# Kernel tuning notes

Hardware: AMD Instinct MI355X
Metric: run time of the kernel (lower is better)

Reference implementation:

```python
import jax, jax.numpy as jnp
import numpy as np

B, N, GN, GS = 16, 100000, 4096, 64  # batch, points, num_groups, group_size


def setup_inputs() -> dict:
    key = jax.random.key(0)
    k1, k2, k3 = jax.random.split(key, 3)
    x_proto = jax.random.normal(k1, (B, N, 3), dtype=jnp.float32)
    template = jax.random.normal(k2, (N, 3), dtype=jnp.float32)
    groups = jax.random.randint(k3, (GN, GS), 0, N, dtype=jnp.int32)
    return {"x_proto": x_proto, "template": template, "groups": groups}


def reference(x_proto, template, groups):
    # x_proto: [B, N, 3], template: [N, 3], groups: [GN, GS] int indices
    b, n, _ = x_proto.shape
    Yg = template[groups]                      # [GN, GS, 3] gathered template
    Xg = x_proto[:, groups]                    # [B, GN, GS, 3] gathered current points

    # Kabsch: align template group Y to current X (R @ Y + t ~ X)
    muY = Yg.mean(axis=1)                      # [GN, 3]
    muX = Xg.mean(axis=2)                      # [B, GN, 3]
    Yc = Yg - muY[:, None, :]
    Xc = Xg - muX[:, :, None, :]
    H = jnp.einsum('gni,bgnj->bgij', Yc, Xc)   # [B, GN, 3, 3] covariance
    U, S, Vh = jnp.linalg.svd(H)
    V = jnp.swapaxes(Vh, -2, -1)
    R0 = V @ jnp.swapaxes(U, -2, -1)
    det = jnp.linalg.det(R0)                   # [B, GN]
    # flip last column of V where det < 0 to get a proper rotation
    s = jnp.where(det < 0, -1.0, 1.0).astype(x_proto.dtype)
    col_scale = jnp.stack([jnp.ones_like(s), jnp.ones_like(s), s], axis=-1)  # [B, GN, 3]
    R = (V * col_scale[..., None, :]) @ jnp.swapaxes(U, -2, -1)              # [B, GN, 3, 3]
    t = muX - jnp.einsum('bgij,gj->bgi', R, muY)                             # [B, GN, 3]

    # project template group through (R, t)
    Xg_proj = jnp.einsum('bgij,gnj->bgni', R, Yg) + t[:, :, None, :]         # [B, GN, GS, 3]

    # scatter-add with overlap counting, then average
    flat_idx = groups.reshape(-1)              # [GN*GS]
    out = jnp.zeros_like(x_proto).at[:, flat_idx].add(Xg_proj.reshape(b, -1, 3))
    counts = jnp.zeros((n,), dtype=x_proto.dtype).at[flat_idx].add(1.0)
    counts = jnp.maximum(counts, 1.0)
    return out / counts[None, :, None]
```

## Files before the change

kernel.cpp:

```cpp
#include <hip/hip_runtime.h>
#include <math.h>

static constexpr int BB = 16;
static constexpr int NN = 100000;
static constexpr int GN = 4096;
static constexpr int GS = 64;
static constexpr int NP = BB * GN;
static constexpr int NE = GN * GS;
static constexpr int NBLK = (NN + 255) / 256;

__device__ __forceinline__ float wsum64(float v) {
#pragma unroll
  for (int off = 32; off > 0; off >>= 1) v += __shfl_xor(v, off, 64);
  return v;
}

__global__ __launch_bounds__(256) void k_xpad(
    const float4* __restrict__ x, const float4* __restrict__ tpl,
    float4* __restrict__ x4, float4* __restrict__ tpl4,
    int4* __restrict__ cnt4, int* __restrict__ gtotal) {
  int t = blockIdx.x * 256 + threadIdx.x;
  if (t == 0) *gtotal = 0;
  if (t < NN / 4) {
    cnt4[t] = make_int4(0, 0, 0, 0);
    float4 a = tpl[t * 3 + 0], b = tpl[t * 3 + 1], c = tpl[t * 3 + 2];
    tpl4[t * 4 + 0] = make_float4(a.x, a.y, a.z, 0.f);
    tpl4[t * 4 + 1] = make_float4(a.w, b.x, b.y, 0.f);
    tpl4[t * 4 + 2] = make_float4(b.z, b.w, c.x, 0.f);
    tpl4[t * 4 + 3] = make_float4(c.y, c.z, c.w, 0.f);
  }
  if (t >= BB * NN / 4) return;
  float4 a = x[t * 3 + 0], b = x[t * 3 + 1], c = x[t * 3 + 2];
  x4[t * 4 + 0] = make_float4(a.x, a.y, a.z, 0.f);
  x4[t * 4 + 1] = make_float4(a.w, b.x, b.y, 0.f);
  x4[t * 4 + 2] = make_float4(b.z, b.w, c.x, 0.f);
  x4[t * 4 + 3] = make_float4(c.y, c.z, c.w, 0.f);
}

__global__ __launch_bounds__(256) void k_tpl(
    const float4* __restrict__ tpl4, const int* __restrict__ groups,
    float* __restrict__ Yg, float* __restrict__ GmY, int* __restrict__ cnt) {
  int g    = blockIdx.x * 4 + (threadIdx.x >> 6);
  int lane = threadIdx.x & 63;
  int idx = groups[g * GS + lane];
  atomicAdd(&cnt[idx], 1);
  float4 y = tpl4[idx];
  float* o = Yg + ((size_t)g * GS + lane) * 3;
  o[0] = y.x; o[1] = y.y; o[2] = y.z;
  float sy0 = wsum64(y.x), sy1 = wsum64(y.y), sy2 = wsum64(y.z);
  if (lane == 0) {
    const float inv = 1.0f / 64.0f;
    *(float4*)(GmY + (size_t)g * 4) =
        make_float4(sy0 * inv, sy1 * inv, sy2 * inv, 0.0f);
  }
}

__global__ __launch_bounds__(256) void k_stats(
    const float4* __restrict__ x4, const float* __restrict__ Yg,
    const float* __restrict__ GmY, const int* __restrict__ groups,
    float* __restrict__ Ht) {
  int bid  = (blockIdx.x & 7) * 512 + (blockIdx.x >> 3);
  int wid4 = bid * 4 + (threadIdx.x >> 6);
  int lane = threadIdx.x & 63;
  int s    = lane >> 4;
  int l4   = lane & 15;
  int p = wid4 * 4 + s;
  int b = p >> 12;
  int g = p & (GN - 1);

  int4 iv = *(const int4*)(groups + (size_t)g * GS + l4 * 4);
  const float4* yv = (const float4*)(Yg + ((size_t)g * GS + l4 * 4) * 3);
  float4 ya = yv[0], yb = yv[1], yc = yv[2];

  const float4* xb4 = x4 + (size_t)b * NN;
  float sx0 = 0.f, sx1 = 0.f, sx2 = 0.f;
  float h00 = 0.f, h01 = 0.f, h02 = 0.f;
  float h10 = 0.f, h11 = 0.f, h12 = 0.f;
  float h20 = 0.f, h21 = 0.f, h22 = 0.f;

#define ACC(Y0, Y1, Y2, IDX)                                   \
  {                                                            \
    float4 xv = xb4[IDX];                                      \
    sx0 += xv.x; sx1 += xv.y; sx2 += xv.z;                     \
    h00 += (Y0) * xv.x; h01 += (Y0) * xv.y; h02 += (Y0) * xv.z;\
    h10 += (Y1) * xv.x; h11 += (Y1) * xv.y; h12 += (Y1) * xv.z;\
    h20 += (Y2) * xv.x; h21 += (Y2) * xv.y; h22 += (Y2) * xv.z;\
  }
  ACC(ya.x, ya.y, ya.z, iv.x);
  ACC(ya.w, yb.x, yb.y, iv.y);
  ACC(yb.z, yb.w, yc.x, iv.z);
  ACC(yc.y, yc.z, yc.w, iv.w);
#undef ACC

#define RED(V)                                                 \
  V += __shfl_xor(V, 8, 64); V += __shfl_xor(V, 4, 64);        \
  V += __shfl_xor(V, 2, 64); V += __shfl_xor(V, 1, 64);
  RED(sx0) RED(sx1) RED(sx2)
  RED(h00) RED(h01) RED(h02)
  RED(h10) RED(h11) RED(h12)
  RED(h20) RED(h21) RED(h22)
#undef RED

  if (l4 == 0) {
    const float inv = 1.0f / 64.0f;
    float4 m = *(const float4*)(GmY + (size_t)g * 4);
    float mx0 = sx0 * inv, mx1 = sx1 * inv, mx2 = sx2 * inv;
    float4 o0 = make_float4(mx0, mx1, mx2, h00 - m.x * sx0);
    float4 o1 = make_float4(h01 - m.x * sx1, h02 - m.x * sx2,
                            h10 - m.y * sx0, h11 - m.y * sx1);
    float4 o2 = make_float4(h12 - m.y * sx2, h20 - m.z * sx0,
                            h21 - m.z * sx1, h22 - m.z * sx2);
    float* o = Ht + (size_t)p * 12;
    *(float4*)(o + 0) = o0;
    *(float4*)(o + 4) = o1;
    *(float4*)(o + 8) = o2;
  }
}

#define JROT(P, Q, RR)                                                        \
  {                                                                           \
    float apq = K[P][Q];                                                      \
    if (fabsf(apq) > 1e-30f) {                                                \
      float app = K[P][P], aqq = K[Q][Q];                                     \
      float tau = (aqq - app) / (2.0f * apq);                                 \
      float tt = copysignf(1.0f, tau) / (fabsf(tau) + sqrtf(1.0f + tau*tau)); \
      float cc = 1.0f / sqrtf(1.0f + tt * tt);                                \
      float ss = tt * cc;                                                     \
      K[P][P] = app - tt * apq;                                               \
      K[Q][Q] = aqq + tt * apq;                                               \
      K[P][Q] = 0.0f; K[Q][P] = 0.0f;                                         \
      float krp = K[RR][P], krq = K[RR][Q];                                   \
      K[RR][P] = cc * krp - ss * krq; K[P][RR] = K[RR][P];                    \
      K[RR][Q] = ss * krp + cc * krq; K[Q][RR] = K[RR][Q];                    \
      float v0p = V[0][P], v0q = V[0][Q];                                     \
      float v1p = V[1][P], v1q = V[1][Q];                                     \
      float v2p = V[2][P], v2q = V[2][Q];                                     \
      V[0][P] = cc * v0p - ss * v0q; V[0][Q] = ss * v0p + cc * v0q;           \
      V[1][P] = cc * v1p - ss * v1q; V[1][Q] = ss * v1p + cc * v1q;           \
      V[2][P] = cc * v2p - ss * v2q; V[2][Q] = ss * v2p + cc * v2q;           \
    }                                                                         \
  }

#define FIN(AA, BBi, CC)                                                      \
  {                                                                           \
    float va0 = V[0][AA], va1 = V[1][AA], va2 = V[2][AA];                     \
    float vb0 = V[0][BBi], vb1 = V[1][BBi], vb2 = V[2][BBi];                  \
    float vc0 = V[0][CC], vc1 = V[1][CC], vc2 = V[2][CC];                     \
    float ua0 = A[0][0]*va0 + A[0][1]*va1 + A[0][2]*va2;                      \
    float ua1 = A[1][0]*va0 + A[1][1]*va1 + A[1][2]*va2;                      \
    float ua2 = A[2][0]*va0 + A[2][1]*va1 + A[2][2]*va2;                      \
    float il = 1.0f / sqrtf(ua0*ua0 + ua1*ua1 + ua2*ua2 + 1e-30f);            \
    ua0 *= il; ua1 *= il; ua2 *= il;                                          \
    float ub0 = A[0][0]*vb0 + A[0][1]*vb1 + A[0][2]*vb2;                      \
    float ub1 = A[1][0]*vb0 + A[1][1]*vb1 + A[1][2]*vb2;                      \
    float ub2 = A[2][0]*vb0 + A[2][1]*vb1 + A[2][2]*vb2;                      \
    il = 1.0f / sqrtf(ub0*ub0 + ub1*ub1 + ub2*ub2 + 1e-30f);                  \
    ub0 *= il; ub1 *= il; ub2 *= il;                                          \
    float dd = ua0*ub0 + ua1*ub1 + ua2*ub2;                                   \
    ub0 -= dd * ua0; ub1 -= dd * ua1; ub2 -= dd * ua2;                        \
    il = 1.0f / sqrtf(ub0*ub0 + ub1*ub1 + ub2*ub2 + 1e-30f);                  \
    ub0 *= il; ub1 *= il; ub2 *= il;                                          \
    float uc0 = ua1*ub2 - ua2*ub1;                                            \
    float uc1 = ua2*ub0 - ua0*ub2;                                            \
    float uc2 = ua0*ub1 - ua1*ub0;                                            \
    R[0][0] = va0*ua0 + vb0*ub0 + dsg*vc0*uc0;                                \
    R[0][1] = va0*ua1 + vb0*ub1 + dsg*vc0*uc1;                                \
    R[0][2] = va0*ua2 + vb0*ub2 + dsg*vc0*uc2;                                \
    R[1][0] = va1*ua0 + vb1*ub0 + dsg*vc1*uc0;                                \
    R[1][1] = va1*ua1 + vb1*ub1 + dsg*vc1*uc1;                                \
    R[1][2] = va1*ua2 + vb1*ub2 + dsg*vc1*uc2;                                \
    R[2][0] = va2*ua0 + vb2*ub0 + dsg*vc2*uc0;                                \
    R[2][1] = va2*ua1 + vb2*ub1 + dsg*vc2*uc1;                                \
    R[2][2] = va2*ua2 + vb2*ub2 + dsg*vc2*uc2;                                \
  }

__global__ __launch_bounds__(256) void k_svd(
    const float* __restrict__ Ht, const float* __restrict__ GmY,
    float* __restrict__ Rt) {
  int p = blockIdx.x * 256 + threadIdx.x;
  if (p >= NP) return;
  int g = p & (GN - 1);
  const float* h = Ht + (size_t)p * 12;
  float4 f0 = *(const float4*)(h + 0);
  float4 f1 = *(const float4*)(h + 4);
  float4 f2 = *(const float4*)(h + 8);
  float4 m  = *(const float4*)(GmY + (size_t)g * 4);
  float mx0 = f0.x, mx1 = f0.y, mx2 = f0.z;
  float my0 = m.x, my1 = m.y, my2 = m.z;
  float A[3][3];
  A[0][0] = f0.w; A[0][1] = f1.x; A[0][2] = f1.y;
  A[1][0] = f1.z; A[1][1] = f1.w; A[1][2] = f2.x;
  A[2][0] = f2.y; A[2][1] = f2.z; A[2][2] = f2.w;

  float K[3][3];
#pragma unroll
  for (int i = 0; i < 3; ++i)
#pragma unroll
    for (int j = 0; j < 3; ++j)
      K[i][j] = A[0][i]*A[0][j] + A[1][i]*A[1][j] + A[2][i]*A[2][j];

  float V[3][3] = {{1.f,0.f,0.f},{0.f,1.f,0.f},{0.f,0.f,1.f}};
#pragma unroll
  for (int sweep = 0; sweep < 5; ++sweep) {
    JROT(0, 1, 2);
    JROT(0, 2, 1);
    JROT(1, 2, 0);
  }

  float d0 = K[0][0], d1 = K[1][1], d2 = K[2][2];
  float detV = V[0][0]*(V[1][1]*V[2][2] - V[1][2]*V[2][1])
             - V[0][1]*(V[1][0]*V[2][2] - V[1][2]*V[2][0])
             + V[0][2]*(V[1][0]*V[2][1] - V[1][1]*V[2][0]);
  float dsg = (detV < 0.0f) ? -1.0f : 1.0f;

  float R[3][3];
  if (d0 <= d1 && d0 <= d2) {
    FIN(1, 2, 0);
  } else if (d1 <= d0 && d1 <= d2) {
    FIN(2, 0, 1);
  } else {
    FIN(0, 1, 2);
  }

  float t0 = mx0 - (R[0][0]*my0 + R[0][1]*my1 + R[0][2]*my2);
  float t1 = mx1 - (R[1][0]*my0 + R[1][1]*my1 + R[1][2]*my2);
  float t2 = mx2 - (R[2][0]*my0 + R[2][1]*my1 + R[2][2]*my2);

  float* o = Rt + (size_t)p * 16;
  *(float4*)(o + 0) = make_float4(R[0][0], R[0][1], R[0][2], R[1][0]);
  *(float4*)(o + 4) = make_float4(R[1][1], R[1][2], R[2][0], R[2][1]);
  *(float4*)(o + 8) = make_float4(R[2][2], t0, t1, t2);
}

__global__ __launch_bounds__(256) void k_alloc(
    const int* __restrict__ cnt, int* __restrict__ gtotal,
    int2* __restrict__ rs_cnt, int* __restrict__ cursor) {
  int t = blockIdx.x * 256 + threadIdx.x;
  int lane = threadIdx.x & 63;
  int v = (t < NN) ? cnt[t] : 0;
  int sc = v;
#pragma unroll
  for (int off = 1; off < 64; off <<= 1) {
    int u = __shfl_up(sc, off, 64);
    if (lane >= off) sc += u;
  }
  int wtotal = __shfl(sc, 63, 64);
  int base = 0;
  if (lane == 63) base = atomicAdd(gtotal, wtotal);
  base = __shfl(base, 63, 64);
  if (t < NN) {
    rs_cnt[t] = make_int2(base + sc - v, v);
    cursor[t] = 0;
  }
}

__global__ __launch_bounds__(256) void k_fill(
    const int* __restrict__ groups, const int2* __restrict__ rs_cnt,
    int* __restrict__ cursor, int* __restrict__ entries) {
  int e = blockIdx.x * 256 + threadIdx.x;
  if (e >= NE) return;
  int n = groups[e];
  int pos = atomicAdd(&cursor[n], 1);
  entries[rs_cnt[n].x + pos] = e >> 6;
}

__global__ __launch_bounds__(256) void k_gather(
    const float4* __restrict__ tpl4, const int2* __restrict__ rs_cnt,
    const int* __restrict__ entries, const float* __restrict__ Rt,
    float* __restrict__ out) {
  int n = blockIdx.x * 256 + threadIdx.x;
  if (n >= NN) return;
  int b = blockIdx.y;
  int2 rc = rs_cnt[n];
  int s = rc.x, c = rc.y;
  float4 y = tpl4[n];
  float p0 = 0.f, p1 = 0.f, p2 = 0.f;
  const float* Rb = Rt + (size_t)b * GN * 16;
  for (int j = 0; j < c; ++j) {
    int g = entries[s + j];
    const float* rt = Rb + (size_t)g * 16;
    float4 r0 = *(const float4*)(rt + 0);
    float4 r1 = *(const float4*)(rt + 4);
    float4 r2 = *(const float4*)(rt + 8);
    p0 += r0.x * y.x + r0.y * y.y + r0.z * y.z + r2.y;
    p1 += r0.w * y.x + r1.x * y.y + r1.y * y.z + r2.z;
    p2 += r1.z * y.x + r1.w * y.y + r2.x * y.z + r2.w;
  }
  float inv = 1.0f / fmaxf((float)c, 1.0f);
  float* o = out + ((size_t)b * NN + (size_t)n) * 3;
  o[0] = p0 * inv;
  o[1] = p1 * inv;
  o[2] = p2 * inv;
}

extern "C" void kernel_launch(void* const* d_in, const int* in_sizes, int n_in,
                              void* d_out, int out_size, void* d_ws, size_t ws_size,
                              hipStream_t stream) {
  const float* x      = (const float*)d_in[0];
  const float* tpl    = (const float*)d_in[1];
  const int*   groups = (const int*)d_in[2];
  float* out = (float*)d_out;

  char* ws = (char*)d_ws;
  size_t o_x4   = 0;
  size_t o_tpl4 = o_x4 + 25600000;
  size_t o_yg   = o_tpl4 + 1600000;
  size_t o_ht   = o_yg + 3145728;
  size_t o_rt   = o_ht + 3145728;
  size_t o_gmy  = o_rt + 4194304;
  size_t o_cnt  = o_gmy + 65536;
  size_t o_rsc  = o_cnt + 400000;
  size_t o_cur  = o_rsc + 800000;
  size_t o_gt   = o_cur + 400000;
  size_t o_ent  = o_gt + 64;
  float* x4     = (float*)(ws + o_x4);
  float* tpl4   = (float*)(ws + o_tpl4);
  float* Yg     = (float*)(ws + o_yg);
  float* Ht     = (float*)(ws + o_ht);
  float* Rt     = (float*)(ws + o_rt);
  float* GmY    = (float*)(ws + o_gmy);
  int*   cnt    = (int*)(ws + o_cnt);
  int2*  rs_cnt = (int2*)(ws + o_rsc);
  int*   cursor = (int*)(ws + o_cur);
  int*   gtotal = (int*)(ws + o_gt);
  int*   entries= (int*)(ws + o_ent);

  k_xpad<<<(BB * NN / 4 + 255) / 256, 256, 0, stream>>>(
      (const float4*)x, (const float4*)tpl, (float4*)x4, (float4*)tpl4,
      (int4*)cnt, gtotal);
  k_tpl<<<GN / 4, 256, 0, stream>>>((const float4*)tpl4, groups, Yg, GmY, cnt);
  k_stats<<<NP / 16, 256, 0, stream>>>((const float4*)x4, Yg, GmY, groups, Ht);
  k_svd<<<NP / 256, 256, 0, stream>>>(Ht, GmY, Rt);
  k_alloc<<<NBLK, 256, 0, stream>>>(cnt, gtotal, rs_cnt, cursor);
  k_fill<<<NE / 256, 256, 0, stream>>>(groups, rs_cnt, cursor, entries);
  k_gather<<<dim3(NBLK, BB), 256, 0, stream>>>(
      (const float4*)tpl4, rs_cnt, entries, Rt, out);
}
```

Measured before the change: 138.0 us.

## Store per-group transforms as quaternions and remap gather threads across batch

The SVD kernel now turns each rotation into a unit quaternion plus translation packed in 8 floats instead of 12-of-16, halving the per-group transform record the gather kernel reads. The gather kernel maps 16 batch entries of one point to adjacent threads, so entries and template loads are shared across the batch, and rotates using the quaternion formula. This cuts gather-side memory traffic but adds conversion arithmetic, rounding differences from the quaternion round-trip, and uncoalesced strided output writes across batches.

```diff
diff --git a/kernel.cpp b/kernel.cpp
--- a/kernel.cpp
+++ b/kernel.cpp
@@ -176,7 +176,7 @@
 
 __global__ __launch_bounds__(256) void k_svd(
     const float* __restrict__ Ht, const float* __restrict__ GmY,
-    float* __restrict__ Rt) {
+    float* __restrict__ Qt) {
   int p = blockIdx.x * 256 + threadIdx.x;
   if (p >= NP) return;
   int g = p & (GN - 1);
@@ -226,10 +226,39 @@
   float t1 = mx1 - (R[1][0]*my0 + R[1][1]*my1 + R[1][2]*my2);
   float t2 = mx2 - (R[2][0]*my0 + R[2][1]*my1 + R[2][2]*my2);
 
-  float* o = Rt + (size_t)p * 16;
-  *(float4*)(o + 0) = make_float4(R[0][0], R[0][1], R[0][2], R[1][0]);
-  *(float4*)(o + 4) = make_float4(R[1][1], R[1][2], R[2][0], R[2][1]);
-  *(float4*)(o + 8) = make_float4(R[2][2], t0, t1, t2);
+  float qw, qx, qy, qz;
+  float tr = R[0][0] + R[1][1] + R[2][2];
+  if (tr > 0.f) {
+    float S = sqrtf(tr + 1.0f) * 2.0f;
+    qw = 0.25f * S;
+    qx = (R[2][1] - R[1][2]) / S;
+    qy = (R[0][2] - R[2][0]) / S;
+    qz = (R[1][0] - R[0][1]) / S;
+  } else if (R[0][0] > R[1][1] && R[0][0] > R[2][2]) {
+    float S = sqrtf(1.0f + R[0][0] - R[1][1] - R[2][2]) * 2.0f;
+    qw = (R[2][1] - R[1][2]) / S;
+    qx = 0.25f * S;
+    qy = (R[0][1] + R[1][0]) / S;
+    qz = (R[0][2] + R[2][0]) / S;
+  } else if (R[1][1] > R[2][2]) {
+    float S = sqrtf(1.0f + R[1][1] - R[0][0] - R[2][2]) * 2.0f;
+    qw = (R[0][2] - R[2][0]) / S;
+    qx = (R[0][1] + R[1][0]) / S;
+    qy = 0.25f * S;
+    qz = (R[1][2] + R[2][1]) / S;
+  } else {
+    float S = sqrtf(1.0f + R[2][2] - R[0][0] - R[1][1]) * 2.0f;
+    qw = (R[1][0] - R[0][1]) / S;
+    qx = (R[0][2] + R[2][0]) / S;
+    qy = (R[1][2] + R[2][1]) / S;
+    qz = 0.25f * S;
+  }
+  float il2 = 1.0f / sqrtf(qw*qw + qx*qx + qy*qy + qz*qz);
+  qw *= il2; qx *= il2; qy *= il2; qz *= il2;
+
+  float* o = Qt + (size_t)p * 8;
+  *(float4*)(o + 0) = make_float4(qx, qy, qz, qw);
+  *(float4*)(o + 4) = make_float4(t0, t1, t2, 0.f);
 }
 
 __global__ __launch_bounds__(256) void k_alloc(
@@ -266,31 +295,32 @@
 
 __global__ __launch_bounds__(256) void k_gather(
     const float4* __restrict__ tpl4, const int2* __restrict__ rs_cnt,
-    const int* __restrict__ entries, const float* __restrict__ Rt,
+    const int* __restrict__ entries, const float* __restrict__ Qt,
     float* __restrict__ out) {
-  int n = blockIdx.x * 256 + threadIdx.x;
+  int nl = threadIdx.x >> 4;
+  int b  = threadIdx.x & 15;
+  int n  = blockIdx.x * 16 + nl;
   if (n >= NN) return;
-  int b = blockIdx.y;
   int2 rc = rs_cnt[n];
   int s = rc.x, c = rc.y;
   float4 y = tpl4[n];
   float p0 = 0.f, p1 = 0.f, p2 = 0.f;
-  const float* Rb = Rt + (size_t)b * GN * 16;
+  const float* Qb = Qt + (size_t)b * GN * 8;
   for (int j = 0; j < c; ++j) {
     int g = entries[s + j];
-    const float* rt = Rb + (size_t)g * 16;
-    float4 r0 = *(const float4*)(rt + 0);
-    float4 r1 = *(const float4*)(rt + 4);
-    float4 r2 = *(const float4*)(rt + 8);
-    p0 += r0.x * y.x + r0.y * y.y + r0.z * y.z + r2.y;
-    p1 += r0.w * y.x + r1.x * y.y + r1.y * y.z + r2.z;
-    p2 += r1.z * y.x + r1.w * y.y + r2.x * y.z + r2.w;
+    const float* qt = Qb + (size_t)g * 8;
+    float4 q = *(const float4*)(qt + 0);
+    float4 tv = *(const float4*)(qt + 4);
+    float tx = 2.f * (q.y * y.z - q.z * y.y);
+    float ty = 2.f * (q.z * y.x - q.x * y.z);
+    float tz = 2.f * (q.x * y.y - q.y * y.x);
+    p0 += y.x + q.w * tx + (q.y * tz - q.z * ty) + tv.x;
+    p1 += y.y + q.w * ty + (q.z * tx - q.x * tz) + tv.y;
+    p2 += y.z + q.w * tz + (q.x * ty - q.y * tx) + tv.z;
   }
   float inv = 1.0f / fmaxf((float)c, 1.0f);
   float* o = out + ((size_t)b * NN + (size_t)n) * 3;
-  o[0] = p0 * inv;
-  o[1] = p1 * inv;
-  o[2] = p2 * inv;
+  *(float3*)o = make_float3(p0 * inv, p1 * inv, p2 * inv);
 }
 
 extern "C" void kernel_launch(void* const* d_in, const int* in_sizes, int n_in,
@@ -306,8 +336,8 @@
   size_t o_tpl4 = o_x4 + 25600000;
   size_t o_yg   = o_tpl4 + 1600000;
   size_t o_ht   = o_yg + 3145728;
-  size_t o_rt   = o_ht + 3145728;
-  size_t o_gmy  = o_rt + 4194304;
+  size_t o_qt   = o_ht + 3145728;
+  size_t o_gmy  = o_qt + 2097152;
   size_t o_cnt  = o_gmy + 65536;
   size_t o_rsc  = o_cnt + 400000;
   size_t o_cur  = o_rsc + 800000;
@@ -317,7 +347,7 @@
   float* tpl4   = (float*)(ws + o_tpl4);
   float* Yg     = (float*)(ws + o_yg);
   float* Ht     = (float*)(ws + o_ht);
-  float* Rt     = (float*)(ws + o_rt);
+  float* Qt     = (float*)(ws + o_qt);
   float* GmY    = (float*)(ws + o_gmy);
   int*   cnt    = (int*)(ws + o_cnt);
   int2*  rs_cnt = (int2*)(ws + o_rsc);
@@ -330,9 +360,9 @@
       (int4*)cnt, gtotal);
   k_tpl<<<GN / 4, 256, 0, stream>>>((const float4*)tpl4, groups, Yg, GmY, cnt);
   k_stats<<<NP / 16, 256, 0, stream>>>((const float4*)x4, Yg, GmY, groups, Ht);
-  k_svd<<<NP / 256, 256, 0, stream>>>(Ht, GmY, Rt);
+  k_svd<<<NP / 256, 256, 0, stream>>>(Ht, GmY, Qt);
   k_alloc<<<NBLK, 256, 0, stream>>>(cnt, gtotal, rs_cnt, cursor);
   k_fill<<<NE / 256, 256, 0, stream>>>(groups, rs_cnt, cursor, entries);
-  k_gather<<<dim3(NBLK, BB), 256, 0, stream>>>(
-      (const float4*)tpl4, rs_cnt, entries, Rt, out);
-}
+  k_gather<<<(NN + 15) / 16, 256, 0, stream>>>(
+      (const float4*)tpl4, rs_cnt, entries, Qt, out);
+}
```

New measurement: 134.8 us. -2.3%, faster.
